# Kernel tuning notes

Measured on AMD Instinct MI355X. Metric: run time of the kernel, lower is better.

The kernel has to match this reference:

```python
import jax, jax.numpy as jnp
import numpy as np

# Dimensions: B jets, P max particles, C coords, F features, K neighbors,
# H hidden units, O MLP output dim. Edge feature dim E = 2*(C+F).
B, P, C, F, K, H, O = 256, 128, 2, 7, 16, 128, 256
E = 2 * (C + F)
BIG = 1e9  # distance assigned to invalid (padded) neighbors


def setup_inputs() -> dict:
    key = jax.random.key(0)
    k1, k2, k3, k4 = jax.random.split(key, 4)
    raw = jax.random.normal(k1, (B, P, C + F), dtype=jnp.float32)
    # per-jet particle counts in [K+2, P]; padding is contiguous at the end
    lengths = jax.random.randint(k2, (B,), K + 2, P + 1)
    mask = (jnp.arange(P)[None, :] < lengths[:, None]).astype(jnp.float32)  # [B,P]
    # zero out padded rows and append mask as the last column (as the layer expects)
    x = jnp.concatenate([raw * mask[..., None], mask[..., None]], axis=-1)  # [B,P,C+F+1]
    W1 = jax.random.normal(k3, (E, H), dtype=jnp.float32) * (1.0 / np.sqrt(E))
    b1 = jnp.zeros((H,), dtype=jnp.float32)
    W2 = jax.random.normal(k4, (H, O), dtype=jnp.float32) * (1.0 / np.sqrt(H))
    b2 = jnp.zeros((O,), dtype=jnp.float32)
    return {"x": x, "W1": W1, "b1": b1, "W2": W2, "b2": b2}


def reference(x, W1, b1, W2, b2):
    coords = x[..., :C]          # [B,P,C]
    feats = x[..., C:-1]         # [B,P,F]
    mask = x[..., -1]            # [B,P] 1=real particle, 0=padding
    valid = mask > 0

    # --- kNN on coordinates (masked, vectorized over jets) ---
    diff = coords[:, :, None, :] - coords[:, None, :, :]      # [B,P,P,C]
    # squared distance: same ordering as tf.norm, avoids sqrt-at-zero issues
    dist2 = jnp.sum(diff * diff, axis=-1)                      # [B,P,P]
    dist2 = jnp.where(valid[:, None, :], dist2, BIG)           # mask padded neighbors
    _, idx = jax.lax.top_k(-dist2, K + 1)                      # [B,P,K+1]
    idx = idx[..., 1:]                                         # drop self -> [B,P,K]

    # --- gather neighbor coords/features ---
    idx_flat = idx.reshape(B, P * K)
    nbr_c = jnp.take_along_axis(coords, idx_flat[..., None], axis=1).reshape(B, P, K, C)
    nbr_f = jnp.take_along_axis(feats, idx_flat[..., None], axis=1).reshape(B, P, K, F)
    ctr_c = jnp.broadcast_to(coords[:, :, None, :], (B, P, K, C))
    ctr_f = jnp.broadcast_to(feats[:, :, None, :], (B, P, K, F))

    # edge features: [coord_i, feat_i, coord_j - coord_i, feat_j - feat_i]
    edge = jnp.concatenate([ctr_c, ctr_f, nbr_c - ctr_c, nbr_f - ctr_f], axis=-1)  # [B,P,K,E]

    # --- MLP + mean aggregation over neighbors ---
    h = jax.nn.relu(edge @ W1 + b1)   # [B,P,K,H]
    h = jax.nn.relu(h @ W2 + b2)      # [B,P,K,O]
    avg = jnp.mean(h, axis=2)         # [B,P,O]

    # append mask column; zero out padded particles (matches _fix_number_of_particles)
    out = jnp.concatenate([avg, jnp.ones((B, P, 1), avg.dtype)], axis=-1) * mask[..., None]
    return out
```

## Files before the change

kernel.cpp:

```cpp
#include <hip/hip_runtime.h>

#define BB 256
#define PP 128
#define CC 2
#define FF 7
#define KK 16
#define HH 128
#define OO 256
#define EE 18
#define XCH 10
#define BIGD 1000000000.0f
#define GPT 4

typedef __bf16 bf16x8 __attribute__((ext_vector_type(8)));
typedef __bf16 bf16x4 __attribute__((ext_vector_type(4)));
typedef float  f32x4  __attribute__((ext_vector_type(4)));

__global__ __launch_bounds__(256) void pack_w_kernel(const float* __restrict__ W1,
                                                     const float* __restrict__ W2,
                                                     __bf16* __restrict__ W2p,
                                                     __bf16* __restrict__ W1p) {
    const int t = blockIdx.x * 256 + threadIdx.x;
    if (t < 32768) {
        const int j  = t & 7;
        const int l  = (t >> 3) & 63;
        const int ks = (t >> 9) & 3;
        const int ct = t >> 11;
        const int row = ks * 32 + ((l >> 4) * 8) + j;
        const int col = ct * 16 + (l & 15);
        W2p[t] = (__bf16)W2[row * OO + col];
    } else {
        const int t2 = t - 32768;
        const int j  = t2 & 7;
        const int l  = (t2 >> 3) & 63;
        const int nt = t2 >> 9;
        const int k  = ((l >> 4) * 8) + j;
        const int n  = nt * 16 + (l & 15);
        W1p[t2] = (k < EE) ? (__bf16)W1[k * HH + n] : (__bf16)0.0f;
    }
}

__global__ __launch_bounds__(256, 4) void mlp_kernel(const float* __restrict__ x,
                                                     const __bf16* __restrict__ W1p,
                                                     const float* __restrict__ b1,
                                                     const __bf16* __restrict__ W2p,
                                                     const float* __restrict__ b2,
                                                     float* __restrict__ out) {
    __shared__ __bf16 sh1A[16 * 64 * 8];
    __shared__ float  sb1[HH];
    __shared__ float  sb2[OO];
    __shared__ float  smask[GPT];
    __shared__ int    sknn[GPT][KK];

    const int tid = threadIdx.x;
    const int lane = tid & 63;
    const int w = tid >> 6;
    const int quad = lane >> 4;
    const int lcol = lane & 15;

    const int pbase = blockIdx.x * GPT;
    const int bidx = pbase >> 7;
    const int i0 = pbase & (PP - 1);
    const float* xb = x + (size_t)bidx * PP * XCH;
    float* outrow = out + (size_t)pbase * (OO + 1);

    if (tid < HH) sb1[tid] = b1[tid];
    sb2[tid] = b2[tid];
    if (tid < GPT) smask[tid] = xb[(i0 + tid) * XCH + (XCH - 1)];
    __syncthreads();

    const bool allmasked =
        (smask[0] == 0.0f) & (smask[1] == 0.0f) & (smask[2] == 0.0f) & (smask[3] == 0.0f);
    if (allmasked) {
        for (int o = tid; o < GPT * (OO + 1); o += 256) outrow[o] = 0.0f;
        return;
    }

    const int i = i0 + w;
    const float cix = xb[i * XCH + 0];
    const float ciy = xb[i * XCH + 1];

    const int j0 = lane, j1 = lane + 64;
    float d0, d1;
    {
        const float2 c0 = *(const float2*)(xb + j0 * XCH);
        const float m0 = xb[j0 * XCH + (XCH - 1)];
        float dx = cix - c0.x, dy = ciy - c0.y;
        d0 = __fadd_rn(__fmul_rn(dx, dx), __fmul_rn(dy, dy));
        if (m0 <= 0.0f || j0 == i) d0 = BIGD;
    }
    {
        const float2 c1 = *(const float2*)(xb + j1 * XCH);
        const float m1 = xb[j1 * XCH + (XCH - 1)];
        float dx = cix - c1.x, dy = ciy - c1.y;
        d1 = __fadd_rn(__fmul_rn(dx, dx), __fmul_rn(dy, dy));
        if (m1 <= 0.0f || j1 == i) d1 = BIGD;
    }

    const unsigned d0b = __float_as_uint(d0);
    const unsigned d1b = __float_as_uint(d1);

    unsigned long long A0 = ~0ull, A1 = ~0ull, W0 = 0ull, W1 = 0ull;
    int need = KK;

    auto step = [&](unsigned long long m0, unsigned long long m1) {
        const unsigned long long z0 = A0 & m0;
        const unsigned long long z1 = A1 & m1;
        const int c = __popcll(z0) + __popcll(z1);
        if (c == need) { W0 |= z0; W1 |= z1; A0 = A1 = 0ull; need = 0; }
        else if (c > need) { A0 = z0; A1 = z1; }
        else { W0 |= z0; W1 |= z1; need -= c; A0 &= ~z0; A1 &= ~z1; }
    };

#pragma unroll 1
    for (int bp = 30; bp >= 0; --bp) {
        if (need == 0) break;
        const unsigned long long m0 = __ballot(((d0b >> bp) & 1u) == 0u);
        const unsigned long long m1 = __ballot(((d1b >> bp) & 1u) == 0u);
        step(m0, m1);
    }
    if (need) step(~0ull, 0ull);
    {
        const unsigned long long M5 = 0x00000000FFFFFFFFull;
        const unsigned long long M4 = 0x0000FFFF0000FFFFull;
        const unsigned long long M3 = 0x00FF00FF00FF00FFull;
        const unsigned long long M2 = 0x0F0F0F0F0F0F0F0Full;
        const unsigned long long M1 = 0x3333333333333333ull;
        const unsigned long long M0 = 0x5555555555555555ull;
        if (need) step(M5, M5);
        if (need) step(M4, M4);
        if (need) step(M3, M3);
        if (need) step(M2, M2);
        if (need) step(M1, M1);
        if (need) step(M0, M0);
    }
    W0 |= A0; W1 |= A1;

    unsigned int mb0 = __builtin_amdgcn_mbcnt_lo((unsigned)(W0 & 0xffffffffull), 0u);
    mb0 = __builtin_amdgcn_mbcnt_hi((unsigned)(W0 >> 32), mb0);
    unsigned int mb1 = __builtin_amdgcn_mbcnt_lo((unsigned)(W1 & 0xffffffffull), 0u);
    mb1 = __builtin_amdgcn_mbcnt_hi((unsigned)(W1 >> 32), mb1);
    const int base1 = __popcll(W0);

    if ((W0 >> lane) & 1ull) sknn[w][mb0] = j0;
    if ((W1 >> lane) & 1ull) sknn[w][base1 + mb1] = j1;
    __syncthreads();

    const int jn = sknn[w][lcol];
    const float* ci = xb + i * XCH;
    const float* cj = xb + jn * XCH;
    const float2 a01 = *(const float2*)(ci + 0);
    const float2 a23 = *(const float2*)(ci + 2);
    const float2 a45 = *(const float2*)(ci + 4);
    const float2 a67 = *(const float2*)(ci + 6);
    const float  a8  = ci[8];
    const float2 n01 = *(const float2*)(cj + 0);
    const float2 n23 = *(const float2*)(cj + 2);
    const float2 n45 = *(const float2*)(cj + 4);
    const float2 n67 = *(const float2*)(cj + 6);
    const float  n8  = cj[8];

    float v[8];
#pragma unroll
    for (int e = 0; e < 8; ++e) v[e] = 0.0f;
    if (quad == 0) {
        v[0] = a01.x; v[1] = a01.y; v[2] = a23.x; v[3] = a23.y;
        v[4] = a45.x; v[5] = a45.y; v[6] = a67.x; v[7] = a67.y;
    } else if (quad == 1) {
        v[0] = a8;
        v[1] = n01.x - a01.x; v[2] = n01.y - a01.y;
        v[3] = n23.x - a23.x; v[4] = n23.y - a23.y;
        v[5] = n45.x - a45.x; v[6] = n45.y - a45.y;
        v[7] = n67.x - a67.x;
    } else if (quad == 2) {
        v[0] = n67.y - a67.y;
        v[1] = n8 - a8;
    }

    bf16x8 ef;
#pragma unroll
    for (int e = 0; e < 8; ++e) ef[e] = (__bf16)v[e];

    bf16x8 wf[8];
#pragma unroll
    for (int nt = 0; nt < 8; ++nt)
        wf[nt] = *(const bf16x8*)&W1p[(size_t)((nt * 64 + lane) * 8)];

    const f32x4 z4 = {0.0f, 0.0f, 0.0f, 0.0f};
    f32x4 h[8];
#pragma unroll
    for (int nt = 0; nt < 8; ++nt)
        h[nt] = __builtin_amdgcn_mfma_f32_16x16x32_bf16(wf[nt], ef, z4, 0, 0, 0);

#pragma unroll
    for (int nt = 0; nt < 8; ++nt) {
        const int ks = nt >> 1;
        const int lp = (((nt * 2 + (quad >> 1)) & 3) << 4) | lcol;
        bf16x4 hv;
#pragma unroll
        for (int r = 0; r < 4; ++r) {
            const int m = nt * 16 + quad * 4 + r;
            hv[r] = (__bf16)fmaxf(h[nt][r] + sb1[m], 0.0f);
        }
        *(bf16x4*)&sh1A[((ks * 4 + w) * 64 + lp) * 8 + (quad & 1) * 4] = hv;
    }
    __syncthreads();

    f32x4 acc[GPT][4];
#pragma unroll
    for (int g = 0; g < GPT; ++g)
#pragma unroll
        for (int ct = 0; ct < 4; ++ct) acc[g][ct] = z4;

#pragma unroll
    for (int ks = 0; ks < 4; ++ks) {
        bf16x8 af[GPT], bfr[4];
#pragma unroll
        for (int g = 0; g < GPT; ++g)
            af[g] = *(const bf16x8*)&sh1A[((ks * 4 + g) * 64 + lane) * 8];
#pragma unroll
        for (int ct = 0; ct < 4; ++ct)
            bfr[ct] = *(const bf16x8*)&W2p[(size_t)((((w * 4 + ct) * 4 + ks) * 64 + lane) * 8)];
#pragma unroll
        for (int g = 0; g < GPT; ++g)
#pragma unroll
            for (int ct = 0; ct < 4; ++ct)
                acc[g][ct] = __builtin_amdgcn_mfma_f32_16x16x32_bf16(
                    af[g], bfr[ct], acc[g][ct], 0, 0, 0);
    }

    float val[4];
#pragma unroll
    for (int g = 0; g < GPT; ++g) {
#pragma unroll
        for (int ct = 0; ct < 4; ++ct) {
            const int col = w * 64 + ct * 16 + lcol;
            const float bc = sb2[col];
            float s = 0.0f;
#pragma unroll
            for (int r = 0; r < 4; ++r) s += fmaxf(acc[g][ct][r] + bc, 0.0f);
            s += __shfl_xor(s, 16, 64);
            s += __shfl_xor(s, 32, 64);
            if (quad == g) val[ct] = s;
        }
    }
    const float m = smask[quad] * (1.0f / KK);
#pragma unroll
    for (int ct = 0; ct < 4; ++ct)
        outrow[(size_t)quad * (OO + 1) + w * 64 + ct * 16 + lcol] = val[ct] * m;
    if (tid < GPT) outrow[(size_t)tid * (OO + 1) + OO] = smask[tid];
}

extern "C" void kernel_launch(void* const* d_in, const int* in_sizes, int n_in,
                              void* d_out, int out_size, void* d_ws, size_t ws_size,
                              hipStream_t stream) {
    const float* x  = (const float*)d_in[0];
    const float* W1 = (const float*)d_in[1];
    const float* b1 = (const float*)d_in[2];
    const float* W2 = (const float*)d_in[3];
    const float* b2 = (const float*)d_in[4];
    float* out = (float*)d_out;

    __bf16* W2p = (__bf16*)d_ws;
    __bf16* W1p = (__bf16*)((char*)d_ws + 65536);

    pack_w_kernel<<<144, 256, 0, stream>>>(W1, W2, W2p, W1p);

    const int nblocks = (BB * PP) / GPT;
    mlp_kernel<<<nblocks, 256, 0, stream>>>(x, W1p, b1, W2p, b2, out);
}
```

Before: 129.5 us.

## Process eight particles per 512-thread block and skip kNN for masked particles

Each block now handles eight particles, one per wave, and every wave computes two output column tiles across all eight particles in the second GEMM. This halves the W2 fragment loads per particle and gives each wave more MFMAs per B-fragment load. Waves whose particle is padded now skip the kNN ballot search and write dummy neighbor indices. The cost is a larger block, more shared memory, and fewer blocks, which could reduce occupancy and scheduling flexibility.

Measured after the change: 135.3 us. 1.05x slower.

```diff
diff --git a/kernel.cpp b/kernel.cpp
--- a/kernel.cpp
+++ b/kernel.cpp
@@ -10,7 +10,7 @@
 #define EE 18
 #define XCH 10
 #define BIGD 1000000000.0f
-#define GPT 4
+#define NPB 8
 
 typedef __bf16 bf16x8 __attribute__((ext_vector_type(8)));
 typedef __bf16 bf16x4 __attribute__((ext_vector_type(4)));
@@ -40,17 +40,17 @@
     }
 }
 
-__global__ __launch_bounds__(256, 4) void mlp_kernel(const float* __restrict__ x,
+__global__ __launch_bounds__(512, 4) void mlp_kernel(const float* __restrict__ x,
                                                      const __bf16* __restrict__ W1p,
                                                      const float* __restrict__ b1,
                                                      const __bf16* __restrict__ W2p,
                                                      const float* __restrict__ b2,
                                                      float* __restrict__ out) {
-    __shared__ __bf16 sh1A[16 * 64 * 8];
+    __shared__ __bf16 sh1A[4 * NPB * 64 * 8];
     __shared__ float  sb1[HH];
     __shared__ float  sb2[OO];
-    __shared__ float  smask[GPT];
-    __shared__ int    sknn[GPT][KK];
+    __shared__ float  smask[NPB];
+    __shared__ int    sknn[NPB][KK];
 
     const int tid = threadIdx.x;
     const int lane = tid & 63;
@@ -58,92 +58,97 @@
     const int quad = lane >> 4;
     const int lcol = lane & 15;
 
-    const int pbase = blockIdx.x * GPT;
+    const int pbase = blockIdx.x * NPB;
     const int bidx = pbase >> 7;
     const int i0 = pbase & (PP - 1);
     const float* xb = x + (size_t)bidx * PP * XCH;
     float* outrow = out + (size_t)pbase * (OO + 1);
 
     if (tid < HH) sb1[tid] = b1[tid];
-    sb2[tid] = b2[tid];
-    if (tid < GPT) smask[tid] = xb[(i0 + tid) * XCH + (XCH - 1)];
+    if (tid < OO) sb2[tid] = b2[tid];
+    if (tid < NPB) smask[tid] = xb[(i0 + tid) * XCH + (XCH - 1)];
     __syncthreads();
 
-    const bool allmasked =
-        (smask[0] == 0.0f) & (smask[1] == 0.0f) & (smask[2] == 0.0f) & (smask[3] == 0.0f);
-    if (allmasked) {
-        for (int o = tid; o < GPT * (OO + 1); o += 256) outrow[o] = 0.0f;
+    bool anylive = false;
+#pragma unroll
+    for (int g = 0; g < NPB; ++g) anylive |= (smask[g] != 0.0f);
+    if (!anylive) {
+        for (int o = tid; o < NPB * (OO + 1); o += 512) outrow[o] = 0.0f;
         return;
     }
 
     const int i = i0 + w;
-    const float cix = xb[i * XCH + 0];
-    const float ciy = xb[i * XCH + 1];
-
-    const int j0 = lane, j1 = lane + 64;
-    float d0, d1;
-    {
-        const float2 c0 = *(const float2*)(xb + j0 * XCH);
-        const float m0 = xb[j0 * XCH + (XCH - 1)];
-        float dx = cix - c0.x, dy = ciy - c0.y;
-        d0 = __fadd_rn(__fmul_rn(dx, dx), __fmul_rn(dy, dy));
-        if (m0 <= 0.0f || j0 == i) d0 = BIGD;
-    }
-    {
-        const float2 c1 = *(const float2*)(xb + j1 * XCH);
-        const float m1 = xb[j1 * XCH + (XCH - 1)];
-        float dx = cix - c1.x, dy = ciy - c1.y;
-        d1 = __fadd_rn(__fmul_rn(dx, dx), __fmul_rn(dy, dy));
-        if (m1 <= 0.0f || j1 == i) d1 = BIGD;
-    }
-
-    const unsigned d0b = __float_as_uint(d0);
-    const unsigned d1b = __float_as_uint(d1);
-
-    unsigned long long A0 = ~0ull, A1 = ~0ull, W0 = 0ull, W1 = 0ull;
-    int need = KK;
-
-    auto step = [&](unsigned long long m0, unsigned long long m1) {
-        const unsigned long long z0 = A0 & m0;
-        const unsigned long long z1 = A1 & m1;
-        const int c = __popcll(z0) + __popcll(z1);
-        if (c == need) { W0 |= z0; W1 |= z1; A0 = A1 = 0ull; need = 0; }
-        else if (c > need) { A0 = z0; A1 = z1; }
-        else { W0 |= z0; W1 |= z1; need -= c; A0 &= ~z0; A1 &= ~z1; }
-    };
+    if (smask[w] != 0.0f) {
+        const float cix = xb[i * XCH + 0];
+        const float ciy = xb[i * XCH + 1];
+
+        const int j0 = lane, j1 = lane + 64;
+        float d0, d1;
+        {
+            const float2 c0 = *(const float2*)(xb + j0 * XCH);
+            const float m0 = xb[j0 * XCH + (XCH - 1)];
+            float dx = cix - c0.x, dy = ciy - c0.y;
+            d0 = __fadd_rn(__fmul_rn(dx, dx), __fmul_rn(dy, dy));
+            if (m0 <= 0.0f || j0 == i) d0 = BIGD;
+        }
+        {
+            const float2 c1 = *(const float2*)(xb + j1 * XCH);
+            const float m1 = xb[j1 * XCH + (XCH - 1)];
+            float dx = cix - c1.x, dy = ciy - c1.y;
+            d1 = __fadd_rn(__fmul_rn(dx, dx), __fmul_rn(dy, dy));
+            if (m1 <= 0.0f || j1 == i) d1 = BIGD;
+        }
+
+        const unsigned d0b = __float_as_uint(d0);
+        const unsigned d1b = __float_as_uint(d1);
+
+        unsigned long long A0 = ~0ull, A1 = ~0ull, W0 = 0ull, W1 = 0ull;
+        int need = KK;
+
+        auto step = [&](unsigned long long m0, unsigned long long m1) {
+            const unsigned long long z0 = A0 & m0;
+            const unsigned long long z1 = A1 & m1;
+            const int c = __popcll(z0) + __popcll(z1);
+            if (c == need) { W0 |= z0; W1 |= z1; A0 = A1 = 0ull; need = 0; }
+            else if (c > need) { A0 = z0; A1 = z1; }
+            else { W0 |= z0; W1 |= z1; need -= c; A0 &= ~z0; A1 &= ~z1; }
+        };
 
 #pragma unroll 1
-    for (int bp = 30; bp >= 0; --bp) {
-        if (need == 0) break;
-        const unsigned long long m0 = __ballot(((d0b >> bp) & 1u) == 0u);
-        const unsigned long long m1 = __ballot(((d1b >> bp) & 1u) == 0u);
-        step(m0, m1);
-    }
-    if (need) step(~0ull, 0ull);
-    {
-        const unsigned long long M5 = 0x00000000FFFFFFFFull;
-        const unsigned long long M4 = 0x0000FFFF0000FFFFull;
-        const unsigned long long M3 = 0x00FF00FF00FF00FFull;
-        const unsigned long long M2 = 0x0F0F0F0F0F0F0F0Full;
-        const unsigned long long M1 = 0x3333333333333333ull;
-        const unsigned long long M0 = 0x5555555555555555ull;
-        if (need) step(M5, M5);
-        if (need) step(M4, M4);
-        if (need) step(M3, M3);
-        if (need) step(M2, M2);
-        if (need) step(M1, M1);
-        if (need) step(M0, M0);
-    }
-    W0 |= A0; W1 |= A1;
-
-    unsigned int mb0 = __builtin_amdgcn_mbcnt_lo((unsigned)(W0 & 0xffffffffull), 0u);
-    mb0 = __builtin_amdgcn_mbcnt_hi((unsigned)(W0 >> 32), mb0);
-    unsigned int mb1 = __builtin_amdgcn_mbcnt_lo((unsigned)(W1 & 0xffffffffull), 0u);
-    mb1 = __builtin_amdgcn_mbcnt_hi((unsigned)(W1 >> 32), mb1);
-    const int base1 = __popcll(W0);
-
-    if ((W0 >> lane) & 1ull) sknn[w][mb0] = j0;
-    if ((W1 >> lane) & 1ull) sknn[w][base1 + mb1] = j1;
+        for (int bp = 30; bp >= 0; --bp) {
+            if (need == 0) break;
+            const unsigned long long m0 = __ballot(((d0b >> bp) & 1u) == 0u);
+            const unsigned long long m1 = __ballot(((d1b >> bp) & 1u) == 0u);
+            step(m0, m1);
+        }
+        if (need) step(~0ull, 0ull);
+        {
+            const unsigned long long M5 = 0x00000000FFFFFFFFull;
+            const unsigned long long M4 = 0x0000FFFF0000FFFFull;
+            const unsigned long long M3 = 0x00FF00FF00FF00FFull;
+            const unsigned long long M2 = 0x0F0F0F0F0F0F0F0Full;
+            const unsigned long long M1 = 0x3333333333333333ull;
+            const unsigned long long M0 = 0x5555555555555555ull;
+            if (need) step(M5, M5);
+            if (need) step(M4, M4);
+            if (need) step(M3, M3);
+            if (need) step(M2, M2);
+            if (need) step(M1, M1);
+            if (need) step(M0, M0);
+        }
+        W0 |= A0; W1 |= A1;
+
+        unsigned int mb0 = __builtin_amdgcn_mbcnt_lo((unsigned)(W0 & 0xffffffffull), 0u);
+        mb0 = __builtin_amdgcn_mbcnt_hi((unsigned)(W0 >> 32), mb0);
+        unsigned int mb1 = __builtin_amdgcn_mbcnt_lo((unsigned)(W1 & 0xffffffffull), 0u);
+        mb1 = __builtin_amdgcn_mbcnt_hi((unsigned)(W1 >> 32), mb1);
+        const int base1 = __popcll(W0);
+
+        if ((W0 >> lane) & 1ull) sknn[w][mb0] = j0;
+        if ((W1 >> lane) & 1ull) sknn[w][base1 + mb1] = j1;
+    } else {
+        if (lane < KK) sknn[w][lane] = 0;
+    }
     __syncthreads();
 
     const int jn = sknn[w][lcol];
@@ -202,53 +207,56 @@
             const int m = nt * 16 + quad * 4 + r;
             hv[r] = (__bf16)fmaxf(h[nt][r] + sb1[m], 0.0f);
         }
-        *(bf16x4*)&sh1A[((ks * 4 + w) * 64 + lp) * 8 + (quad & 1) * 4] = hv;
+        *(bf16x4*)&sh1A[((ks * NPB + w) * 64 + lp) * 8 + (quad & 1) * 4] = hv;
     }
     __syncthreads();
 
-    f32x4 acc[GPT][4];
-#pragma unroll
-    for (int g = 0; g < GPT; ++g)
-#pragma unroll
-        for (int ct = 0; ct < 4; ++ct) acc[g][ct] = z4;
+    f32x4 acc[NPB][2];
+#pragma unroll
+    for (int g = 0; g < NPB; ++g) {
+        acc[g][0] = z4; acc[g][1] = z4;
+    }
 
 #pragma unroll
     for (int ks = 0; ks < 4; ++ks) {
-        bf16x8 af[GPT], bfr[4];
-#pragma unroll
-        for (int g = 0; g < GPT; ++g)
-            af[g] = *(const bf16x8*)&sh1A[((ks * 4 + g) * 64 + lane) * 8];
-#pragma unroll
-        for (int ct = 0; ct < 4; ++ct)
-            bfr[ct] = *(const bf16x8*)&W2p[(size_t)((((w * 4 + ct) * 4 + ks) * 64 + lane) * 8)];
-#pragma unroll
-        for (int g = 0; g < GPT; ++g)
-#pragma unroll
-            for (int ct = 0; ct < 4; ++ct)
-                acc[g][ct] = __builtin_amdgcn_mfma_f32_16x16x32_bf16(
-                    af[g], bfr[ct], acc[g][ct], 0, 0, 0);
-    }
-
-    float val[4];
-#pragma unroll
-    for (int g = 0; g < GPT; ++g) {
-#pragma unroll
-        for (int ct = 0; ct < 4; ++ct) {
-            const int col = w * 64 + ct * 16 + lcol;
+        bf16x8 bfr[2];
+#pragma unroll
+        for (int ctl = 0; ctl < 2; ++ctl) {
+            const int ctg = w * 2 + ctl;
+            bfr[ctl] = *(const bf16x8*)&W2p[(size_t)(((ctg * 4 + ks) * 64 + lane) * 8)];
+        }
+#pragma unroll
+        for (int g = 0; g < NPB; ++g) {
+            const bf16x8 af = *(const bf16x8*)&sh1A[((ks * NPB + g) * 64 + lane) * 8];
+            acc[g][0] = __builtin_amdgcn_mfma_f32_16x16x32_bf16(af, bfr[0], acc[g][0], 0, 0, 0);
+            acc[g][1] = __builtin_amdgcn_mfma_f32_16x16x32_bf16(af, bfr[1], acc[g][1], 0, 0, 0);
+        }
+    }
+
+    float val[2][2];
+#pragma unroll
+    for (int g = 0; g < NPB; ++g) {
+#pragma unroll
+        for (int ctl = 0; ctl < 2; ++ctl) {
+            const int col = (w * 2 + ctl) * 16 + lcol;
             const float bc = sb2[col];
             float s = 0.0f;
 #pragma unroll
-            for (int r = 0; r < 4; ++r) s += fmaxf(acc[g][ct][r] + bc, 0.0f);
+            for (int r = 0; r < 4; ++r) s += fmaxf(acc[g][ctl][r] + bc, 0.0f);
             s += __shfl_xor(s, 16, 64);
             s += __shfl_xor(s, 32, 64);
-            if (quad == g) val[ct] = s;
-        }
-    }
-    const float m = smask[quad] * (1.0f / KK);
-#pragma unroll
-    for (int ct = 0; ct < 4; ++ct)
-        outrow[(size_t)quad * (OO + 1) + w * 64 + ct * 16 + lcol] = val[ct] * m;
-    if (tid < GPT) outrow[(size_t)tid * (OO + 1) + OO] = smask[tid];
+            if (quad == (g & 3)) val[g >> 2][ctl] = s;
+        }
+    }
+#pragma unroll
+    for (int hh = 0; hh < 2; ++hh) {
+        const int g = quad + 4 * hh;
+        const float m = smask[g] * (1.0f / KK);
+#pragma unroll
+        for (int ctl = 0; ctl < 2; ++ctl)
+            outrow[(size_t)g * (OO + 1) + (w * 2 + ctl) * 16 + lcol] = val[hh][ctl] * m;
+    }
+    if (tid < NPB) outrow[(size_t)tid * (OO + 1) + OO] = smask[tid];
 }
 
 extern "C" void kernel_launch(void* const* d_in, const int* in_sizes, int n_in,
@@ -266,6 +274,6 @@
 
     pack_w_kernel<<<144, 256, 0, stream>>>(W1, W2, W2p, W1p);
 
-    const int nblocks = (BB * PP) / GPT;
-    mlp_kernel<<<nblocks, 256, 0, stream>>>(x, W1p, b1, W2p, b2, out);
+    const int nblocks = (BB * PP) / NPB;
+    mlp_kernel<<<nblocks, 512, 0, stream>>>(x, W1p, b1, W2p, b2, out);
 }
```

## Stage jet particle rows in LDS and skip kNN for masked waves

Applied to the files above, without the earlier changes.

Each block now copies the whole jet's particle array (128x10 floats) into padded shared memory and reads coordinates and features for the distance and edge-feature computation from LDS instead of global memory. The mask check now uses direct global loads instead of a shared-memory round trip, and biases are read from global memory without staging. Waves whose particle is masked skip the kNN bit-select. The aim is fewer scattered global loads and one less barrier, at the cost of a cooperative 5 KB load per block that duplicates work across the 32 blocks sharing a jet.

Measured after the change: 134.7 us. +4.1%, slower.

```diff
diff --git a/kernel.cpp b/kernel.cpp
--- a/kernel.cpp
+++ b/kernel.cpp
@@ -2,8 +2,6 @@
 
 #define BB 256
 #define PP 128
-#define CC 2
-#define FF 7
 #define KK 16
 #define HH 128
 #define OO 256
@@ -11,6 +9,7 @@
 #define XCH 10
 #define BIGD 1000000000.0f
 #define GPT 4
+#define XS 11
 
 typedef __bf16 bf16x8 __attribute__((ext_vector_type(8)));
 typedef __bf16 bf16x4 __attribute__((ext_vector_type(4)));
@@ -46,10 +45,8 @@
                                                      const __bf16* __restrict__ W2p,
                                                      const float* __restrict__ b2,
                                                      float* __restrict__ out) {
+    __shared__ float  sxr[PP * XS];
     __shared__ __bf16 sh1A[16 * 64 * 8];
-    __shared__ float  sb1[HH];
-    __shared__ float  sb2[OO];
-    __shared__ float  smask[GPT];
     __shared__ int    sknn[GPT][KK];
 
     const int tid = threadIdx.x;
@@ -64,122 +61,110 @@
     const float* xb = x + (size_t)bidx * PP * XCH;
     float* outrow = out + (size_t)pbase * (OO + 1);
 
-    if (tid < HH) sb1[tid] = b1[tid];
-    sb2[tid] = b2[tid];
-    if (tid < GPT) smask[tid] = xb[(i0 + tid) * XCH + (XCH - 1)];
-    __syncthreads();
-
-    const bool allmasked =
-        (smask[0] == 0.0f) & (smask[1] == 0.0f) & (smask[2] == 0.0f) & (smask[3] == 0.0f);
-    if (allmasked) {
+    const float m0 = xb[(i0 + 0) * XCH + 9];
+    const float m1 = xb[(i0 + 1) * XCH + 9];
+    const float m2 = xb[(i0 + 2) * XCH + 9];
+    const float m3 = xb[(i0 + 3) * XCH + 9];
+    if (m0 == 0.0f && m1 == 0.0f && m2 == 0.0f && m3 == 0.0f) {
         for (int o = tid; o < GPT * (OO + 1); o += 256) outrow[o] = 0.0f;
         return;
     }
 
+    for (int t = tid; t < PP * XCH; t += 256) {
+        const int r = t / XCH;
+        const int c = t - r * XCH;
+        sxr[r * XS + c] = xb[t];
+    }
+    __syncthreads();
+
     const int i = i0 + w;
-    const float cix = xb[i * XCH + 0];
-    const float ciy = xb[i * XCH + 1];
-
-    const int j0 = lane, j1 = lane + 64;
-    float d0, d1;
-    {
-        const float2 c0 = *(const float2*)(xb + j0 * XCH);
-        const float m0 = xb[j0 * XCH + (XCH - 1)];
-        float dx = cix - c0.x, dy = ciy - c0.y;
-        d0 = __fadd_rn(__fmul_rn(dx, dx), __fmul_rn(dy, dy));
-        if (m0 <= 0.0f || j0 == i) d0 = BIGD;
-    }
-    {
-        const float2 c1 = *(const float2*)(xb + j1 * XCH);
-        const float m1 = xb[j1 * XCH + (XCH - 1)];
-        float dx = cix - c1.x, dy = ciy - c1.y;
-        d1 = __fadd_rn(__fmul_rn(dx, dx), __fmul_rn(dy, dy));
-        if (m1 <= 0.0f || j1 == i) d1 = BIGD;
-    }
-
-    const unsigned d0b = __float_as_uint(d0);
-    const unsigned d1b = __float_as_uint(d1);
-
-    unsigned long long A0 = ~0ull, A1 = ~0ull, W0 = 0ull, W1 = 0ull;
-    int need = KK;
-
-    auto step = [&](unsigned long long m0, unsigned long long m1) {
-        const unsigned long long z0 = A0 & m0;
-        const unsigned long long z1 = A1 & m1;
-        const int c = __popcll(z0) + __popcll(z1);
-        if (c == need) { W0 |= z0; W1 |= z1; A0 = A1 = 0ull; need = 0; }
-        else if (c > need) { A0 = z0; A1 = z1; }
-        else { W0 |= z0; W1 |= z1; need -= c; A0 &= ~z0; A1 &= ~z1; }
-    };
+    const float mw = (w == 0) ? m0 : (w == 1) ? m1 : (w == 2) ? m2 : m3;
+
+    if (mw != 0.0f) {
+        const float cix = sxr[i * XS + 0];
+        const float ciy = sxr[i * XS + 1];
+
+        const int j0 = lane, j1 = lane + 64;
+        float d0, d1;
+        {
+            const float mj = sxr[j0 * XS + 9];
+            const float dx = cix - sxr[j0 * XS + 0];
+            const float dy = ciy - sxr[j0 * XS + 1];
+            d0 = __fadd_rn(__fmul_rn(dx, dx), __fmul_rn(dy, dy));
+            if (mj <= 0.0f || j0 == i) d0 = BIGD;
+        }
+        {
+            const float mj = sxr[j1 * XS + 9];
+            const float dx = cix - sxr[j1 * XS + 0];
+            const float dy = ciy - sxr[j1 * XS + 1];
+            d1 = __fadd_rn(__fmul_rn(dx, dx), __fmul_rn(dy, dy));
+            if (mj <= 0.0f || j1 == i) d1 = BIGD;
+        }
+
+        const unsigned d0b = __float_as_uint(d0);
+        const unsigned d1b = __float_as_uint(d1);
+
+        unsigned long long A0 = ~0ull, A1 = ~0ull, W0 = 0ull, W1 = 0ull;
+        int need = KK;
+
+        auto step = [&](unsigned long long q0, unsigned long long q1) {
+            const unsigned long long z0 = A0 & q0;
+            const unsigned long long z1 = A1 & q1;
+            const int c = __popcll(z0) + __popcll(z1);
+            if (c == need) { W0 |= z0; W1 |= z1; A0 = A1 = 0ull; need = 0; }
+            else if (c > need) { A0 = z0; A1 = z1; }
+            else { W0 |= z0; W1 |= z1; need -= c; A0 &= ~z0; A1 &= ~z1; }
+        };
 
 #pragma unroll 1
-    for (int bp = 30; bp >= 0; --bp) {
-        if (need == 0) break;
-        const unsigned long long m0 = __ballot(((d0b >> bp) & 1u) == 0u);
-        const unsigned long long m1 = __ballot(((d1b >> bp) & 1u) == 0u);
-        step(m0, m1);
-    }
-    if (need) step(~0ull, 0ull);
-    {
-        const unsigned long long M5 = 0x00000000FFFFFFFFull;
-        const unsigned long long M4 = 0x0000FFFF0000FFFFull;
-        const unsigned long long M3 = 0x00FF00FF00FF00FFull;
-        const unsigned long long M2 = 0x0F0F0F0F0F0F0F0Full;
-        const unsigned long long M1 = 0x3333333333333333ull;
-        const unsigned long long M0 = 0x5555555555555555ull;
-        if (need) step(M5, M5);
-        if (need) step(M4, M4);
-        if (need) step(M3, M3);
-        if (need) step(M2, M2);
-        if (need) step(M1, M1);
-        if (need) step(M0, M0);
-    }
-    W0 |= A0; W1 |= A1;
-
-    unsigned int mb0 = __builtin_amdgcn_mbcnt_lo((unsigned)(W0 & 0xffffffffull), 0u);
-    mb0 = __builtin_amdgcn_mbcnt_hi((unsigned)(W0 >> 32), mb0);
-    unsigned int mb1 = __builtin_amdgcn_mbcnt_lo((unsigned)(W1 & 0xffffffffull), 0u);
-    mb1 = __builtin_amdgcn_mbcnt_hi((unsigned)(W1 >> 32), mb1);
-    const int base1 = __popcll(W0);
-
-    if ((W0 >> lane) & 1ull) sknn[w][mb0] = j0;
-    if ((W1 >> lane) & 1ull) sknn[w][base1 + mb1] = j1;
-    __syncthreads();
+        for (int bp = 30; bp >= 0; --bp) {
+            if (need == 0) break;
+            const unsigned long long q0 = __ballot(((d0b >> bp) & 1u) == 0u);
+            const unsigned long long q1 = __ballot(((d1b >> bp) & 1u) == 0u);
+            step(q0, q1);
+        }
+        if (need) step(~0ull, 0ull);
+        {
+            const unsigned long long M5 = 0x00000000FFFFFFFFull;
+            const unsigned long long M4 = 0x0000FFFF0000FFFFull;
+            const unsigned long long M3 = 0x00FF00FF00FF00FFull;
+            const unsigned long long M2 = 0x0F0F0F0F0F0F0F0Full;
+            const unsigned long long M1 = 0x3333333333333333ull;
+            const unsigned long long M0 = 0x5555555555555555ull;
+            if (need) step(M5, M5);
+            if (need) step(M4, M4);
+            if (need) step(M3, M3);
+            if (need) step(M2, M2);
+            if (need) step(M1, M1);
+            if (need) step(M0, M0);
+        }
+        W0 |= A0; W1 |= A1;
+
+        unsigned int mb0 = __builtin_amdgcn_mbcnt_lo((unsigned)(W0 & 0xffffffffull), 0u);
+        mb0 = __builtin_amdgcn_mbcnt_hi((unsigned)(W0 >> 32), mb0);
+        unsigned int mb1 = __builtin_amdgcn_mbcnt_lo((unsigned)(W1 & 0xffffffffull), 0u);
+        mb1 = __builtin_amdgcn_mbcnt_hi((unsigned)(W1 >> 32), mb1);
+        const int base1 = __popcll(W0);
+
+        if ((W0 >> lane) & 1ull) sknn[w][mb0] = j0;
+        if ((W1 >> lane) & 1ull) sknn[w][base1 + mb1] = j1;
+    } else {
+        if (lane < KK) sknn[w][lane] = 0;
+    }
 
     const int jn = sknn[w][lcol];
-    const float* ci = xb + i * XCH;
-    const float* cj = xb + jn * XCH;
-    const float2 a01 = *(const float2*)(ci + 0);
-    const float2 a23 = *(const float2*)(ci + 2);
-    const float2 a45 = *(const float2*)(ci + 4);
-    const float2 a67 = *(const float2*)(ci + 6);
-    const float  a8  = ci[8];
-    const float2 n01 = *(const float2*)(cj + 0);
-    const float2 n23 = *(const float2*)(cj + 2);
-    const float2 n45 = *(const float2*)(cj + 4);
-    const float2 n67 = *(const float2*)(cj + 6);
-    const float  n8  = cj[8];
-
-    float v[8];
-#pragma unroll
-    for (int e = 0; e < 8; ++e) v[e] = 0.0f;
-    if (quad == 0) {
-        v[0] = a01.x; v[1] = a01.y; v[2] = a23.x; v[3] = a23.y;
-        v[4] = a45.x; v[5] = a45.y; v[6] = a67.x; v[7] = a67.y;
-    } else if (quad == 1) {
-        v[0] = a8;
-        v[1] = n01.x - a01.x; v[2] = n01.y - a01.y;
-        v[3] = n23.x - a23.x; v[4] = n23.y - a23.y;
-        v[5] = n45.x - a45.x; v[6] = n45.y - a45.y;
-        v[7] = n67.x - a67.x;
-    } else if (quad == 2) {
-        v[0] = n67.y - a67.y;
-        v[1] = n8 - a8;
-    }
-
     bf16x8 ef;
 #pragma unroll
-    for (int e = 0; e < 8; ++e) ef[e] = (__bf16)v[e];
+    for (int e = 0; e < 8; ++e) {
+        const int c = quad * 8 + e;
+        const int cA = (c < 9) ? c : ((c < 18) ? c - 9 : 0);
+        const int cN = (c >= 9 && c < 18) ? c - 9 : 0;
+        const float rA = sxr[i * XS + cA];
+        const float rN = sxr[jn * XS + cN];
+        float vv = (c < 9) ? rA : (rN - rA);
+        if (c >= 18) vv = 0.0f;
+        ef[e] = (__bf16)vv;
+    }
 
     bf16x8 wf[8];
 #pragma unroll
@@ -194,15 +179,14 @@
 
 #pragma unroll
     for (int nt = 0; nt < 8; ++nt) {
+        const f32x4 bv = *(const f32x4*)&b1[nt * 16 + quad * 4];
         const int ks = nt >> 1;
         const int lp = (((nt * 2 + (quad >> 1)) & 3) << 4) | lcol;
         bf16x4 hv;
 #pragma unroll
-        for (int r = 0; r < 4; ++r) {
-            const int m = nt * 16 + quad * 4 + r;
-            hv[r] = (__bf16)fmaxf(h[nt][r] + sb1[m], 0.0f);
-        }
-        *(bf16x4*)&sh1A[((ks * 4 + w) * 64 + lp) * 8 + (quad & 1) * 4] = hv;
+        for (int r = 0; r < 4; ++r)
+            hv[r] = (__bf16)fmaxf(h[nt][r] + bv[r], 0.0f);
+        *(bf16x4*)&sh1A[((ks * GPT + w) * 64 + lp) * 8 + (quad & 1) * 4] = hv;
     }
     __syncthreads();
 
@@ -217,7 +201,7 @@
         bf16x8 af[GPT], bfr[4];
 #pragma unroll
         for (int g = 0; g < GPT; ++g)
-            af[g] = *(const bf16x8*)&sh1A[((ks * 4 + g) * 64 + lane) * 8];
+            af[g] = *(const bf16x8*)&sh1A[((ks * GPT + g) * 64 + lane) * 8];
 #pragma unroll
         for (int ct = 0; ct < 4; ++ct)
             bfr[ct] = *(const bf16x8*)&W2p[(size_t)((((w * 4 + ct) * 4 + ks) * 64 + lane) * 8)];
@@ -235,7 +219,7 @@
 #pragma unroll
         for (int ct = 0; ct < 4; ++ct) {
             const int col = w * 64 + ct * 16 + lcol;
-            const float bc = sb2[col];
+            const float bc = b2[col];
             float s = 0.0f;
 #pragma unroll
             for (int r = 0; r < 4; ++r) s += fmaxf(acc[g][ct][r] + bc, 0.0f);
@@ -244,11 +228,15 @@
             if (quad == g) val[ct] = s;
         }
     }
-    const float m = smask[quad] * (1.0f / KK);
+    const float mq = (quad == 0) ? m0 : (quad == 1) ? m1 : (quad == 2) ? m2 : m3;
+    const float msc = mq * (1.0f / KK);
 #pragma unroll
     for (int ct = 0; ct < 4; ++ct)
-        outrow[(size_t)quad * (OO + 1) + w * 64 + ct * 16 + lcol] = val[ct] * m;
-    if (tid < GPT) outrow[(size_t)tid * (OO + 1) + OO] = smask[tid];
+        outrow[(size_t)quad * (OO + 1) + w * 64 + ct * 16 + lcol] = val[ct] * msc;
+    if (tid < GPT) {
+        const float mt = (tid == 0) ? m0 : (tid == 1) ? m1 : (tid == 2) ? m2 : m3;
+        outrow[(size_t)tid * (OO + 1) + OO] = mt;
+    }
 }
 
 extern "C" void kernel_launch(void* const* d_in, const int* in_sizes, int n_in,
```

## Use two-bit radix steps with early exit for kNN select; skip padded particles

Applied to the files above, without the earlier changes.

The per-wave kNN radix select now looks at two distance bits per iteration. It uses three ballots per half to split candidates into four buckets. It tracks the size of the active candidate set so it can stop once that set exactly fills the remaining neighbor slots. Waves whose particle is padding skip the selection entirely and write dummy neighbor indices. The block-wide barrier after writing the neighbor list is dropped, since each wave only reads its own row. This trades more ballots per iteration for half as many serial iterations and less branch overhead.

New measurement: 128.7 us. Within noise of the previous version (-0.6%).

```diff
diff --git a/kernel.cpp b/kernel.cpp
--- a/kernel.cpp
+++ b/kernel.cpp
@@ -2,8 +2,6 @@
 
 #define BB 256
 #define PP 128
-#define CC 2
-#define FF 7
 #define KK 16
 #define HH 128
 #define OO 256
@@ -77,74 +75,106 @@
     }
 
     const int i = i0 + w;
-    const float cix = xb[i * XCH + 0];
-    const float ciy = xb[i * XCH + 1];
-
-    const int j0 = lane, j1 = lane + 64;
-    float d0, d1;
-    {
-        const float2 c0 = *(const float2*)(xb + j0 * XCH);
-        const float m0 = xb[j0 * XCH + (XCH - 1)];
-        float dx = cix - c0.x, dy = ciy - c0.y;
-        d0 = __fadd_rn(__fmul_rn(dx, dx), __fmul_rn(dy, dy));
-        if (m0 <= 0.0f || j0 == i) d0 = BIGD;
-    }
-    {
-        const float2 c1 = *(const float2*)(xb + j1 * XCH);
-        const float m1 = xb[j1 * XCH + (XCH - 1)];
-        float dx = cix - c1.x, dy = ciy - c1.y;
-        d1 = __fadd_rn(__fmul_rn(dx, dx), __fmul_rn(dy, dy));
-        if (m1 <= 0.0f || j1 == i) d1 = BIGD;
-    }
-
-    const unsigned d0b = __float_as_uint(d0);
-    const unsigned d1b = __float_as_uint(d1);
-
-    unsigned long long A0 = ~0ull, A1 = ~0ull, W0 = 0ull, W1 = 0ull;
-    int need = KK;
-
-    auto step = [&](unsigned long long m0, unsigned long long m1) {
-        const unsigned long long z0 = A0 & m0;
-        const unsigned long long z1 = A1 & m1;
-        const int c = __popcll(z0) + __popcll(z1);
-        if (c == need) { W0 |= z0; W1 |= z1; A0 = A1 = 0ull; need = 0; }
-        else if (c > need) { A0 = z0; A1 = z1; }
-        else { W0 |= z0; W1 |= z1; need -= c; A0 &= ~z0; A1 &= ~z1; }
-    };
+    if (smask[w] != 0.0f) {
+        const float cix = xb[i * XCH + 0];
+        const float ciy = xb[i * XCH + 1];
+
+        const int j0 = lane, j1 = lane + 64;
+        float d0, d1;
+        {
+            const float2 c0 = *(const float2*)(xb + j0 * XCH);
+            const float m0 = xb[j0 * XCH + (XCH - 1)];
+            float dx = cix - c0.x, dy = ciy - c0.y;
+            d0 = __fadd_rn(__fmul_rn(dx, dx), __fmul_rn(dy, dy));
+            if (m0 <= 0.0f || j0 == i) d0 = BIGD;
+        }
+        {
+            const float2 c1 = *(const float2*)(xb + j1 * XCH);
+            const float m1 = xb[j1 * XCH + (XCH - 1)];
+            float dx = cix - c1.x, dy = ciy - c1.y;
+            d1 = __fadd_rn(__fmul_rn(dx, dx), __fmul_rn(dy, dy));
+            if (m1 <= 0.0f || j1 == i) d1 = BIGD;
+        }
+
+        const unsigned d0b = __float_as_uint(d0);
+        const unsigned d1b = __float_as_uint(d1);
+
+        unsigned long long A0 = ~0ull, A1 = ~0ull, W0 = 0ull, W1 = 0ull;
+        int need = KK;
+        int asz = 2 * 64;
+
+        auto step = [&](unsigned long long q0, unsigned long long q1) {
+            const unsigned long long z0 = A0 & q0;
+            const unsigned long long z1 = A1 & q1;
+            const int c = __popcll(z0) + __popcll(z1);
+            if (c == need) { W0 |= z0; W1 |= z1; A0 = A1 = 0ull; need = 0; }
+            else if (c > need) { A0 = z0; A1 = z1; asz = c; }
+            else { W0 |= z0; W1 |= z1; need -= c; A0 &= ~z0; A1 &= ~z1; asz -= c; }
+        };
 
 #pragma unroll 1
-    for (int bp = 30; bp >= 0; --bp) {
-        if (need == 0) break;
-        const unsigned long long m0 = __ballot(((d0b >> bp) & 1u) == 0u);
-        const unsigned long long m1 = __ballot(((d1b >> bp) & 1u) == 0u);
-        step(m0, m1);
-    }
-    if (need) step(~0ull, 0ull);
-    {
-        const unsigned long long M5 = 0x00000000FFFFFFFFull;
-        const unsigned long long M4 = 0x0000FFFF0000FFFFull;
-        const unsigned long long M3 = 0x00FF00FF00FF00FFull;
-        const unsigned long long M2 = 0x0F0F0F0F0F0F0F0Full;
-        const unsigned long long M1 = 0x3333333333333333ull;
-        const unsigned long long M0 = 0x5555555555555555ull;
-        if (need) step(M5, M5);
-        if (need) step(M4, M4);
-        if (need) step(M3, M3);
-        if (need) step(M2, M2);
-        if (need) step(M1, M1);
-        if (need) step(M0, M0);
-    }
-    W0 |= A0; W1 |= A1;
-
-    unsigned int mb0 = __builtin_amdgcn_mbcnt_lo((unsigned)(W0 & 0xffffffffull), 0u);
-    mb0 = __builtin_amdgcn_mbcnt_hi((unsigned)(W0 >> 32), mb0);
-    unsigned int mb1 = __builtin_amdgcn_mbcnt_lo((unsigned)(W1 & 0xffffffffull), 0u);
-    mb1 = __builtin_amdgcn_mbcnt_hi((unsigned)(W1 >> 32), mb1);
-    const int base1 = __popcll(W0);
-
-    if ((W0 >> lane) & 1ull) sknn[w][mb0] = j0;
-    if ((W1 >> lane) & 1ull) sknn[w][base1 + mb1] = j1;
-    __syncthreads();
+        for (int t = 14; t >= 0; --t) {
+            const unsigned dg0 = (d0b >> (2 * t + 1)) & 3u;
+            const unsigned dg1 = (d1b >> (2 * t + 1)) & 3u;
+            const unsigned long long p0_0  = __ballot(dg0 == 0u);
+            const unsigned long long p1_0  = __ballot(dg1 == 0u);
+            const unsigned long long p0_01 = __ballot(dg0 <= 1u);
+            const unsigned long long p1_01 = __ballot(dg1 <= 1u);
+            const unsigned long long p0_02 = __ballot(dg0 <= 2u);
+            const unsigned long long p1_02 = __ballot(dg1 <= 2u);
+            const unsigned long long z0_0  = A0 & p0_0,  z1_0  = A1 & p1_0;
+            const unsigned long long z0_01 = A0 & p0_01, z1_01 = A1 & p1_01;
+            const unsigned long long z0_02 = A0 & p0_02, z1_02 = A1 & p1_02;
+            const int c0  = __popcll(z0_0)  + __popcll(z1_0);
+            const int c01 = __popcll(z0_01) + __popcll(z1_01);
+            const int c02 = __popcll(z0_02) + __popcll(z1_02);
+            if (c0 >= need) {
+                A0 = z0_0; A1 = z1_0; asz = c0;
+            } else if (c01 >= need) {
+                W0 |= z0_0; W1 |= z1_0; need -= c0;
+                A0 = z0_01 & ~p0_0; A1 = z1_01 & ~p1_0; asz = c01 - c0;
+            } else if (c02 >= need) {
+                W0 |= z0_01; W1 |= z1_01; need -= c01;
+                A0 = z0_02 & ~p0_01; A1 = z1_02 & ~p1_01; asz = c02 - c01;
+            } else {
+                W0 |= z0_02; W1 |= z1_02; need -= c02;
+                A0 &= ~p0_02; A1 &= ~p1_02; asz -= c02;
+            }
+            if (asz == need) { W0 |= A0; W1 |= A1; A0 = A1 = 0ull; need = 0; break; }
+        }
+        if (need) {
+            const unsigned long long q0 = __ballot((d0b & 1u) == 0u);
+            const unsigned long long q1 = __ballot((d1b & 1u) == 0u);
+            step(q0, q1);
+        }
+        if (need) step(~0ull, 0ull);
+        {
+            const unsigned long long M5 = 0x00000000FFFFFFFFull;
+            const unsigned long long M4 = 0x0000FFFF0000FFFFull;
+            const unsigned long long M3 = 0x00FF00FF00FF00FFull;
+            const unsigned long long M2 = 0x0F0F0F0F0F0F0F0Full;
+            const unsigned long long M1 = 0x3333333333333333ull;
+            const unsigned long long M0 = 0x5555555555555555ull;
+            if (need) step(M5, M5);
+            if (need) step(M4, M4);
+            if (need) step(M3, M3);
+            if (need) step(M2, M2);
+            if (need) step(M1, M1);
+            if (need) step(M0, M0);
+        }
+        W0 |= A0; W1 |= A1;
+
+        unsigned int mb0 = __builtin_amdgcn_mbcnt_lo((unsigned)(W0 & 0xffffffffull), 0u);
+        mb0 = __builtin_amdgcn_mbcnt_hi((unsigned)(W0 >> 32), mb0);
+        unsigned int mb1 = __builtin_amdgcn_mbcnt_lo((unsigned)(W1 & 0xffffffffull), 0u);
+        mb1 = __builtin_amdgcn_mbcnt_hi((unsigned)(W1 >> 32), mb1);
+        const int base1 = __popcll(W0);
+
+        if ((W0 >> lane) & 1ull) sknn[w][mb0] = j0;
+        if ((W1 >> lane) & 1ull) sknn[w][base1 + mb1] = j1;
+    } else {
+        if (lane < KK) sknn[w][lane] = 0;
+    }
 
     const int jn = sknn[w][lcol];
     const float* ci = xb + i * XCH;
@@ -202,7 +232,7 @@
             const int m = nt * 16 + quad * 4 + r;
             hv[r] = (__bf16)fmaxf(h[nt][r] + sb1[m], 0.0f);
         }
-        *(bf16x4*)&sh1A[((ks * 4 + w) * 64 + lp) * 8 + (quad & 1) * 4] = hv;
+        *(bf16x4*)&sh1A[((ks * GPT + w) * 64 + lp) * 8 + (quad & 1) * 4] = hv;
     }
     __syncthreads();
 
@@ -217,7 +247,7 @@
         bf16x8 af[GPT], bfr[4];
 #pragma unroll
         for (int g = 0; g < GPT; ++g)
-            af[g] = *(const bf16x8*)&sh1A[((ks * 4 + g) * 64 + lane) * 8];
+            af[g] = *(const bf16x8*)&sh1A[((ks * GPT + g) * 64 + lane) * 8];
 #pragma unroll
         for (int ct = 0; ct < 4; ++ct)
             bfr[ct] = *(const bf16x8*)&W2p[(size_t)((((w * 4 + ct) * 4 + ks) * 64 + lane) * 8)];
```
